# Kernel optimization log

Measured on AMD Instinct MI355X. Metric: run time of the kernel, lower is better.

The kernel has to match this reference:

```python
import jax, jax.numpy as jnp
import numpy as np

N_NODES = 50000
N_EDGES = 1_600_000
IN_DIM = 256
OUT_DIM = 128
NEG_SLOPE = 0.01  # F.leaky_relu default


def setup_inputs() -> dict:
    key = jax.random.key(0)
    k1, k2, k3, k4, k5 = jax.random.split(key, 5)
    x = jax.random.normal(k1, (N_NODES, IN_DIM), dtype=jnp.float32)
    # glorot_init: uniform in [-r, r], r = sqrt(6/(in+out))
    r = np.sqrt(6.0 / (IN_DIM + OUT_DIM)).astype(np.float32)
    weight = jax.random.uniform(k2, (IN_DIM, OUT_DIM), dtype=jnp.float32, minval=-r, maxval=r)
    adj_rows = jax.random.randint(k3, (N_EDGES,), 0, N_NODES, dtype=jnp.int64 if jax.config.jax_enable_x64 else jnp.int32)
    adj_cols = jax.random.randint(k4, (N_EDGES,), 0, N_NODES, dtype=jnp.int64 if jax.config.jax_enable_x64 else jnp.int32)
    adj_vals = jax.random.uniform(k5, (N_EDGES,), dtype=jnp.float32)
    return {"x": x, "weight": weight, "adj_vals": adj_vals,
            "adj_rows": adj_rows, "adj_cols": adj_cols}


def reference(x, weight, adj_vals, adj_rows, adj_cols):
    # h = X @ W : [N, OUT_DIM]
    h = x @ weight
    # sparse adj @ h via edge-list SpMM: out[r] += v * h[c]
    msgs = adj_vals[:, None] * h[adj_cols]            # [E, OUT_DIM]
    agg = jax.ops.segment_sum(msgs, adj_rows, num_segments=N_NODES)
    # leaky_relu epilogue
    return jnp.where(agg >= 0, agg, NEG_SLOPE * agg)
```

## Files before the change

### kernel.cpp

```cpp
#include <hip/hip_runtime.h>
#include <hip/hip_fp16.h>

#define N_NODES 50000
#define N_EDGES 1600000
#define IN_DIM 256
#define OUT_DIM 128
#define NEG_SLOPE 0.01f

#define SB_SH     10
#define SB_ROWS   1024
#define NSB       ((N_NODES + SB_ROWS - 1) / SB_ROWS)
#define SB_CAP    34816
#define PASSB_SPLIT 8
#define PB_ITERS  ((SB_CAP / PASSB_SPLIT + 511) / 512)

#define BIN_SH    5
#define BIN_ROWS  32
#define NBIN      ((N_NODES + BIN_ROWS - 1) / BIN_ROWS)
#define NBIN_PAD  (NSB * (SB_ROWS / BIN_ROWS))
#define CAPB      1280
#define OVF_CAP   65536

#define SCAT_BLOCKS 256
#define CONVW_BLOCKS 8
#define EPB_S (N_EDGES / SCAT_BLOCKS)
#define SCAT_ITERS ((EPB_S + 511) / 512)

typedef _Float16 f16x8 __attribute__((ext_vector_type(8)));
typedef float    f32x4 __attribute__((ext_vector_type(4)));
typedef float    f32x8 __attribute__((ext_vector_type(8)));

__device__ __forceinline__ float lrelu(float v) {
    return v >= 0.f ? v : NEG_SLOPE * v;
}

#define BM 128
#define GEMM_BLOCKS ((N_NODES + BM - 1) / BM)

#define CVT16(lo, hi) do { \
    lo[0]=(_Float16)xr[0].x; lo[1]=(_Float16)xr[0].y; lo[2]=(_Float16)xr[0].z; lo[3]=(_Float16)xr[0].w; \
    lo[4]=(_Float16)xr[1].x; lo[5]=(_Float16)xr[1].y; lo[6]=(_Float16)xr[1].z; lo[7]=(_Float16)xr[1].w; \
    hi[0]=(_Float16)xr[2].x; hi[1]=(_Float16)xr[2].y; hi[2]=(_Float16)xr[2].z; hi[3]=(_Float16)xr[2].w; \
    hi[4]=(_Float16)xr[3].x; hi[5]=(_Float16)xr[3].y; hi[6]=(_Float16)xr[3].z; hi[7]=(_Float16)xr[3].w; \
} while (0)

__global__ __launch_bounds__(256, 2) void gemm_xw_mfma(const float* __restrict__ x,
                                                       const __half* __restrict__ wtl,
                                                       __half* __restrict__ h) {
    __shared__ f16x8 wt8[32 * 128];
    __shared__ f16x8 xs8[2][4][BM];

    const int t    = threadIdx.x;
    const int lane = t & 63;
    const int wv   = t >> 6;
    const int row0 = blockIdx.x * BM;

    {
        const int4* src = (const int4*)wtl;
        int4* dst = (int4*)wt8;
#pragma unroll
        for (int i = 0; i < 16; ++i) dst[i * 256 + t] = src[i * 256 + t];
    }

    const int srow = t >> 1;
    const int skh  = t & 1;
    const int grow = row0 + srow;
    const bool rv  = grow < N_NODES;
    const float* xp = x + (size_t)(rv ? grow : 0) * IN_DIM + skh * 16;

    float4 xr[4];
#pragma unroll
    for (int i = 0; i < 4; ++i)
        xr[i] = rv ? ((const float4*)xp)[i] : make_float4(0.f, 0.f, 0.f, 0.f);
    {
        f16x8 lo, hi;
        CVT16(lo, hi);
        xs8[0][skh * 2 + 0][srow] = lo;
        xs8[0][skh * 2 + 1][srow] = hi;
    }
    __syncthreads();

    f32x4 acc[2][8];
#pragma unroll
    for (int mf = 0; mf < 2; ++mf)
#pragma unroll
        for (int nf = 0; nf < 8; ++nf) acc[mf][nf] = (f32x4){0.f, 0.f, 0.f, 0.f};

    const int kg  = lane >> 4;
    const int l15 = lane & 15;
    const int mb  = (wv << 5) + l15;

#pragma unroll
    for (int ks = 0; ks < 8; ++ks) {
        const int cur = ks & 1;
        if (ks < 7) {
#pragma unroll
            for (int i = 0; i < 4; ++i)
                xr[i] = rv ? ((const float4*)(xp + (ks + 1) * 32))[i]
                           : make_float4(0.f, 0.f, 0.f, 0.f);
        }
        const f16x8 b0 = xs8[cur][kg][mb];
        const f16x8 b1 = xs8[cur][kg][mb + 16];
#pragma unroll
        for (int nf = 0; nf < 8; ++nf) {
            const f16x8 a = wt8[(((ks << 2) | kg) << 7) + (nf << 4) + l15];
            acc[0][nf] = __builtin_amdgcn_mfma_f32_16x16x32_f16(a, b0, acc[0][nf], 0, 0, 0);
            acc[1][nf] = __builtin_amdgcn_mfma_f32_16x16x32_f16(a, b1, acc[1][nf], 0, 0, 0);
        }
        if (ks < 7) {
            f16x8 lo, hi;
            CVT16(lo, hi);
            xs8[cur ^ 1][skh * 2 + 0][srow] = lo;
            xs8[cur ^ 1][skh * 2 + 1][srow] = hi;
            __syncthreads();
        }
    }

    const int rg = lane >> 4;
#pragma unroll
    for (int mf = 0; mf < 2; ++mf) {
        const int m = row0 + (wv << 5) + (mf << 4) + l15;
        if (m < N_NODES) {
            __half* hp = h + (size_t)m * OUT_DIM + (rg << 2);
#pragma unroll
            for (int nf = 0; nf < 8; ++nf) {
                union { ushort4 u; __half f[4]; } o;
                o.f[0] = __float2half(acc[mf][nf][0]);
                o.f[1] = __float2half(acc[mf][nf][1]);
                o.f[2] = __float2half(acc[mf][nf][2]);
                o.f[3] = __float2half(acc[mf][nf][3]);
                *(ushort4*)(hp + (nf << 4)) = o.u;
            }
        }
    }
}

__global__ __launch_bounds__(512) void scatter_coarse(const int* __restrict__ rows,
                                                      const int* __restrict__ cols,
                                                      const float* __restrict__ vals,
                                                      int* __restrict__ sbcur,
                                                      int* __restrict__ ovfcnt,
                                                      int2* __restrict__ cbuf,
                                                      int2* __restrict__ ovfbuf,
                                                      const float* __restrict__ w,
                                                      __half* __restrict__ wtl) {
    if (blockIdx.x >= SCAT_BLOCKS) {
        const int e0 = ((blockIdx.x - SCAT_BLOCKS) * 512 + threadIdx.x) * 8;
        const int k  = e0 >> 7;
        const int n0 = e0 & 127;
        const float4 a = *(const float4*)(w + e0);
        const float4 b = *(const float4*)(w + e0 + 4);
        __half* dst = wtl + ((size_t)((k >> 3) * 128 + n0)) * 8 + (k & 7);
        dst[0]  = __float2half(a.x);
        dst[8]  = __float2half(a.y);
        dst[16] = __float2half(a.z);
        dst[24] = __float2half(a.w);
        dst[32] = __float2half(b.x);
        dst[40] = __float2half(b.y);
        dst[48] = __float2half(b.z);
        dst[56] = __float2half(b.w);
        return;
    }

    __shared__ int lcur[NSB];
    const int t = threadIdx.x;
    const int ebase = blockIdx.x * EPB_S;

    if (t < NSB) lcur[t] = 0;
    __syncthreads();

    int myr[SCAT_ITERS];
#pragma unroll
    for (int k = 0; k < SCAT_ITERS; ++k) {
        const int i = k * 512 + t;
        myr[k] = -1;
        if (i < EPB_S) {
            const int r = rows[ebase + i];
            myr[k] = r;
            atomicAdd(&lcur[r >> SB_SH], 1);
        }
    }
    __syncthreads();

    if (t < NSB) {
        const int c = lcur[t];
        lcur[t] = (c > 0) ? atomicAdd(&sbcur[t], c) : 0;
    }
    __syncthreads();

#pragma unroll
    for (int k = 0; k < SCAT_ITERS; ++k) {
        const int i = k * 512 + t;
        if (i < EPB_S) {
            const int e = ebase + i;
            const int r = myr[k];
            const int sb = r >> SB_SH;
            const int off = atomicAdd(&lcur[sb], 1);
            const int key = (int)(((unsigned)r << 16) | (unsigned)cols[e]);
            const int vb  = __float_as_int(vals[e]);
            if (off < SB_CAP) {
                cbuf[(size_t)sb * SB_CAP + off] = make_int2(key, vb);
            } else {
                const int p = atomicAdd(ovfcnt, 1);
                if (p < OVF_CAP) ovfbuf[p] = make_int2(key, vb);
            }
        }
    }
}

__global__ __launch_bounds__(512) void scatter_fine(const int* __restrict__ sbcur,
                                                    int* __restrict__ fcur,
                                                    int* __restrict__ ovfcnt,
                                                    const int2* __restrict__ cbuf,
                                                    int2* __restrict__ ebuf,
                                                    int2* __restrict__ ovfbuf) {
    __shared__ int lcur[SB_ROWS / BIN_ROWS];
    const int t    = threadIdx.x;
    const int sb   = blockIdx.x / PASSB_SPLIT;
    const int part = blockIdx.x % PASSB_SPLIT;

    const int cnt_sb = min(sbcur[sb], SB_CAP);
    const int chunk  = (cnt_sb + PASSB_SPLIT - 1) / PASSB_SPLIT;
    const int i0 = part * chunk;
    const int i1 = min(i0 + chunk, cnt_sb);

    if (t < 32) lcur[t] = 0;
    __syncthreads();

    int2 rc[PB_ITERS];
#pragma unroll
    for (int k = 0; k < PB_ITERS; ++k) {
        const int i = i0 + k * 512 + t;
        if (i < i1) {
            rc[k] = cbuf[(size_t)sb * SB_CAP + i];
            const unsigned urow = ((unsigned)rc[k].x) >> 16;
            atomicAdd(&lcur[(urow >> BIN_SH) & 31], 1);
        }
    }
    __syncthreads();

    if (t < 32) {
        const int c = lcur[t];
        lcur[t] = (c > 0) ? atomicAdd(&fcur[(sb << 5) + t], c) : 0;
    }
    __syncthreads();

#pragma unroll
    for (int k = 0; k < PB_ITERS; ++k) {
        const int i = i0 + k * 512 + t;
        if (i < i1) {
            const unsigned urow = ((unsigned)rc[k].x) >> 16;
            const int f   = (int)(urow >> BIN_SH);
            const int off = atomicAdd(&lcur[(urow >> BIN_SH) & 31], 1);
            const int key = (rc[k].x & 0xFFFF) | (int)((urow & (BIN_ROWS - 1)) << 16);
            if (off < CAPB) {
                ebuf[(size_t)f * CAPB + off] = make_int2(key, rc[k].y);
            } else {
                const int p = atomicAdd(ovfcnt, 1);
                if (p < OVF_CAP) ovfbuf[p] = rc[k];
            }
        }
    }
}

#define NCLS 256

__global__ __launch_bounds__(512) void sort_gather(const int* __restrict__ fcur,
                                                   const int* __restrict__ ovfcnt,
                                                   const int2* __restrict__ ebuf,
                                                   const int2* __restrict__ ovfbuf,
                                                   const __half* __restrict__ h,
                                                   float* __restrict__ out) {
    __shared__ int2 srec[CAPB];
    __shared__ int  hist[NCLS];
    __shared__ int  pfx[NCLS];
    __shared__ int  rowoff_l[BIN_ROWS + 1];

    const int t    = threadIdx.x;
    const int bin  = blockIdx.x;
    const int wv   = t >> 6;
    const int lane = t & 63;

    const int cnt_all = fcur[bin];
    const int cnt     = cnt_all < CAPB ? cnt_all : CAPB;
    const size_t base = (size_t)bin * CAPB;

    if (t < NCLS) hist[t] = 0;
    __syncthreads();

    for (int i = t; i < cnt; i += 512) {
        const int k = ebuf[base + i].x;
        atomicAdd(&hist[(((k >> 16) & 31) << 3) | ((k & 0xFFFF) >> 13)], 1);
    }
    __syncthreads();

    if (t < NCLS) pfx[t] = hist[t];
    __syncthreads();
    for (int off = 1; off < NCLS; off <<= 1) {
        const int u = (t >= off && t < NCLS) ? pfx[t - off] : 0;
        __syncthreads();
        if (t < NCLS) pfx[t] += u;
        __syncthreads();
    }
    if (t < NCLS) hist[t] = pfx[t] - hist[t];
    if (t < BIN_ROWS) rowoff_l[t] = t ? pfx[(t << 3) - 1] : 0;
    if (t == BIN_ROWS) rowoff_l[BIN_ROWS] = cnt;
    __syncthreads();

    for (int i = t; i < cnt; i += 512) {
        const int2 r = ebuf[base + i];
        const int cls = (((r.x >> 16) & 31) << 3) | ((r.x & 0xFFFF) >> 13);
        const int pos = atomicAdd(&hist[cls], 1);
        srec[pos] = r;
    }
    __syncthreads();

    const int grp = lane >> 4;
    const int gl  = lane & 15;
    int novf = *ovfcnt;
    if (novf > OVF_CAP) novf = OVF_CAP;

    for (int p = 0; p < 2; ++p) {
        const int lr0 = (wv << 2) + 2 * p;
        const int lr1 = lr0 + 1;
        const int b0 = rowoff_l[lr0], e0 = rowoff_l[lr0 + 1];
        const int b1 = rowoff_l[lr1], e1 = rowoff_l[lr1 + 1];
        const int n0 = e0 - b0, n1 = e1 - b1;
        const int nmax = n0 > n1 ? n0 : n1;
        const int iters = (nmax + 3) >> 2;

        f32x8 a0 = (f32x8){0.f,0.f,0.f,0.f,0.f,0.f,0.f,0.f};
        f32x8 a1 = (f32x8){0.f,0.f,0.f,0.f,0.f,0.f,0.f,0.f};

        for (int it = 0; it < iters; ++it) {
            const int i0 = b0 + (it << 2) + grp;
            const int i1 = b1 + (it << 2) + grp;
            const bool v0i = i0 < e0;
            const bool v1i = i1 < e1;
            const int2 rA = srec[v0i ? i0 : 0];
            const int2 rB = srec[v1i ? i1 : 0];
            const float vA = v0i ? __int_as_float(rA.y) : 0.f;
            const float vB = v1i ? __int_as_float(rB.y) : 0.f;
            const f16x8 hA = *(const f16x8*)(h + (size_t)(rA.x & 0xFFFF) * OUT_DIM + (gl << 3));
            const f16x8 hB = *(const f16x8*)(h + (size_t)(rB.x & 0xFFFF) * OUT_DIM + (gl << 3));
#pragma unroll
            for (int j = 0; j < 8; ++j) {
                a0[j] += vA * (float)hA[j];
                a1[j] += vB * (float)hB[j];
            }
        }

        for (int e = 0; e < novf; ++e) {
            const int2 rec = ovfbuf[e];
            const unsigned urow = ((unsigned)rec.x) >> 16;
            if ((int)(urow >> BIN_SH) == bin && grp == 0) {
                const int lrow = (int)(urow & (BIN_ROWS - 1));
                if (lrow == lr0 || lrow == lr1) {
                    const float v = __int_as_float(rec.y);
                    const f16x8 hv = *(const f16x8*)(h + (size_t)(rec.x & 0xFFFF) * OUT_DIM + (gl << 3));
#pragma unroll
                    for (int j = 0; j < 8; ++j) {
                        if (lrow == lr0) a0[j] += v * (float)hv[j];
                        else             a1[j] += v * (float)hv[j];
                    }
                }
            }
        }

#pragma unroll
        for (int j = 0; j < 8; ++j) {
            float x0 = a0[j], x1 = a1[j];
            x0 += __shfl_xor(x0, 16); x0 += __shfl_xor(x0, 32);
            x1 += __shfl_xor(x1, 16); x1 += __shfl_xor(x1, 32);
            a0[j] = x0; a1[j] = x1;
        }

        const int lrow = (grp & 2) ? lr1 : lr0;
        const int grow = (bin << BIN_SH) + lrow;
        float q[4];
#pragma unroll
        for (int k = 0; k < 4; ++k) {
            const float lo = (grp & 2) ? a1[k]     : a0[k];
            const float hi = (grp & 2) ? a1[k + 4] : a0[k + 4];
            q[k] = lrelu((grp & 1) ? hi : lo);
        }
        if (grow < N_NODES) {
            float4 o = make_float4(q[0], q[1], q[2], q[3]);
            *(float4*)(out + (size_t)grow * OUT_DIM + (gl << 3) + ((grp & 1) << 2)) = o;
        }
    }
}

extern "C" void kernel_launch(void* const* d_in, const int* in_sizes, int n_in,
                              void* d_out, int out_size, void* d_ws, size_t ws_size,
                              hipStream_t stream) {
    const float* x    = (const float*)d_in[0];
    const float* w    = (const float*)d_in[1];
    const float* vals = (const float*)d_in[2];
    const int*   rows = (const int*)d_in[3];
    const int*   cols = (const int*)d_in[4];
    float* out = (float*)d_out;

    char* ws = (char*)d_ws;
    size_t off = 0;
    auto alloc = [&](size_t bytes) {
        void* p = ws + off;
        off = (off + bytes + 255) & ~(size_t)255;
        return p;
    };
    int2*  cbuf    = (int2*) alloc((size_t)NSB * SB_CAP * sizeof(int2));
    __half* h      = (__half*)cbuf;
    int2*  ebuf    = (int2*) alloc((size_t)NBIN * CAPB * sizeof(int2));
    int2*  ovfbuf  = (int2*) alloc((size_t)OVF_CAP * sizeof(int2));
    __half* wtl    = (__half*)alloc((size_t)IN_DIM * OUT_DIM * sizeof(__half));
    int*   meta    = (int*)  alloc((size_t)(NSB + NBIN_PAD + 1) * sizeof(int));
    int*   sbcur   = meta;
    int*   fcur    = meta + NSB;
    int*   ovfcnt  = meta + NSB + NBIN_PAD;

    hipMemsetAsync(meta, 0, (size_t)(NSB + NBIN_PAD + 1) * sizeof(int), stream);

    scatter_coarse<<<SCAT_BLOCKS + CONVW_BLOCKS, 512, 0, stream>>>(rows, cols, vals,
                                                                   sbcur, ovfcnt, cbuf, ovfbuf, w, wtl);
    scatter_fine<<<NSB * PASSB_SPLIT, 512, 0, stream>>>(sbcur, fcur, ovfcnt, cbuf, ebuf, ovfbuf);
    gemm_xw_mfma<<<GEMM_BLOCKS, 256, 0, stream>>>(x, wtl, h);
    sort_gather<<<NBIN, 512, 0, stream>>>(fcur, ovfcnt, ebuf, ovfbuf, h, out);
}
```

Baseline: 200.6 us.

## Process four rows per wave with software-prefetched gathers in sort_gather

The sort_gather kernel now stages each bin's edge records in shared memory once instead of reading them from global memory twice. It replaces the block-wide Hillis-Steele scan with a wave-shuffle scan. The gather loop handles all four rows of a wave at once, and the fp16 h-row loads are double-buffered so the next iteration's loads are in flight during the current FMAs. This aims to hide gather latency and cut synchronisation and redundant global reads. In exchange it uses more registers and about 10KB more LDS, under a launch bound of 4 blocks.

```diff
diff --git a/kernel.cpp b/kernel.cpp
--- a/kernel.cpp
+++ b/kernel.cpp
@@ -265,16 +265,29 @@
 
 #define NCLS 256
 
-__global__ __launch_bounds__(512) void sort_gather(const int* __restrict__ fcur,
-                                                   const int* __restrict__ ovfcnt,
-                                                   const int2* __restrict__ ebuf,
-                                                   const int2* __restrict__ ovfbuf,
-                                                   const __half* __restrict__ h,
-                                                   float* __restrict__ out) {
+#define STAGE(IT, HV, VV) do {                                                  \
+    _Pragma("unroll")                                                           \
+    for (int q = 0; q < 4; ++q) {                                               \
+        const int idx = beg[q] + ((IT) << 2) + grp;                             \
+        const bool vld = idx < end[q];                                          \
+        const int2 r = srec[vld ? idx : 0];                                     \
+        VV[q] = vld ? __int_as_float(r.y) : 0.f;                                \
+        HV[q] = *(const f16x8*)(h + (size_t)(r.x & 0xFFFF) * OUT_DIM + (gl << 3)); \
+    }                                                                           \
+} while (0)
+
+__global__ __launch_bounds__(512, 4) void sort_gather(const int* __restrict__ fcur,
+                                                      const int* __restrict__ ovfcnt,
+                                                      const int2* __restrict__ ebuf,
+                                                      const int2* __restrict__ ovfbuf,
+                                                      const __half* __restrict__ h,
+                                                      float* __restrict__ out) {
+    __shared__ int2 urec[CAPB];
     __shared__ int2 srec[CAPB];
     __shared__ int  hist[NCLS];
     __shared__ int  pfx[NCLS];
     __shared__ int  rowoff_l[BIN_ROWS + 1];
+    __shared__ int  wsum[4];
 
     const int t    = threadIdx.x;
     const int bin  = blockIdx.x;
@@ -289,26 +302,41 @@
     __syncthreads();
 
     for (int i = t; i < cnt; i += 512) {
-        const int k = ebuf[base + i].x;
-        atomicAdd(&hist[(((k >> 16) & 31) << 3) | ((k & 0xFFFF) >> 13)], 1);
-    }
-    __syncthreads();
-
-    if (t < NCLS) pfx[t] = hist[t];
-    __syncthreads();
-    for (int off = 1; off < NCLS; off <<= 1) {
-        const int u = (t >= off && t < NCLS) ? pfx[t - off] : 0;
+        const int2 r = ebuf[base + i];
+        urec[i] = r;
+        atomicAdd(&hist[(((r.x >> 16) & 31) << 3) | ((r.x & 0xFFFF) >> 13)], 1);
+    }
+    __syncthreads();
+
+    {
+        const int v = (t < NCLS) ? hist[t] : 0;
+        int s = v;
+#pragma unroll
+        for (int off = 1; off < 64; off <<= 1) {
+            const int u = __shfl_up(s, off);
+            if (lane >= off) s += u;
+        }
+        if (t < NCLS && lane == 63) wsum[wv] = s;
         __syncthreads();
-        if (t < NCLS) pfx[t] += u;
+        if (t == 0) {
+            int a = 0;
+#pragma unroll
+            for (int i = 0; i < 4; ++i) { const int c = wsum[i]; wsum[i] = a; a += c; }
+        }
         __syncthreads();
-    }
-    if (t < NCLS) hist[t] = pfx[t] - hist[t];
+        if (t < NCLS) {
+            const int incl = s + wsum[wv];
+            pfx[t]  = incl;
+            hist[t] = incl - v;
+        }
+    }
+    __syncthreads();
     if (t < BIN_ROWS) rowoff_l[t] = t ? pfx[(t << 3) - 1] : 0;
     if (t == BIN_ROWS) rowoff_l[BIN_ROWS] = cnt;
     __syncthreads();
 
     for (int i = t; i < cnt; i += 512) {
-        const int2 r = ebuf[base + i];
+        const int2 r = urec[i];
         const int cls = (((r.x >> 16) & 31) << 3) | ((r.x & 0xFFFF) >> 13);
         const int pos = atomicAdd(&hist[cls], 1);
         srec[pos] = r;
@@ -317,77 +345,76 @@
 
     const int grp = lane >> 4;
     const int gl  = lane & 15;
+    const int r0  = wv << 2;
+
+    int beg[4], end[4];
+#pragma unroll
+    for (int q = 0; q < 4; ++q) { beg[q] = rowoff_l[r0 + q]; end[q] = rowoff_l[r0 + q + 1]; }
+    int nmax = 0;
+#pragma unroll
+    for (int q = 0; q < 4; ++q) nmax = max(nmax, end[q] - beg[q]);
+    const int iters = (nmax + 3) >> 2;
+
+    f32x8 acc[4];
+#pragma unroll
+    for (int q = 0; q < 4; ++q) acc[q] = (f32x8){0.f,0.f,0.f,0.f,0.f,0.f,0.f,0.f};
+
+    f16x8 hc[4], hn[4];
+    float vc[4], vn[4];
+    if (iters > 0) STAGE(0, hc, vc);
+    for (int it = 0; it < iters; ++it) {
+        if (it + 1 < iters) STAGE(it + 1, hn, vn);
+#pragma unroll
+        for (int q = 0; q < 4; ++q)
+#pragma unroll
+            for (int j = 0; j < 8; ++j) acc[q][j] += vc[q] * (float)hc[q][j];
+#pragma unroll
+        for (int q = 0; q < 4; ++q) { hc[q] = hn[q]; vc[q] = vn[q]; }
+    }
+
     int novf = *ovfcnt;
     if (novf > OVF_CAP) novf = OVF_CAP;
-
-    for (int p = 0; p < 2; ++p) {
-        const int lr0 = (wv << 2) + 2 * p;
-        const int lr1 = lr0 + 1;
-        const int b0 = rowoff_l[lr0], e0 = rowoff_l[lr0 + 1];
-        const int b1 = rowoff_l[lr1], e1 = rowoff_l[lr1 + 1];
-        const int n0 = e0 - b0, n1 = e1 - b1;
-        const int nmax = n0 > n1 ? n0 : n1;
-        const int iters = (nmax + 3) >> 2;
-
-        f32x8 a0 = (f32x8){0.f,0.f,0.f,0.f,0.f,0.f,0.f,0.f};
-        f32x8 a1 = (f32x8){0.f,0.f,0.f,0.f,0.f,0.f,0.f,0.f};
-
-        for (int it = 0; it < iters; ++it) {
-            const int i0 = b0 + (it << 2) + grp;
-            const int i1 = b1 + (it << 2) + grp;
-            const bool v0i = i0 < e0;
-            const bool v1i = i1 < e1;
-            const int2 rA = srec[v0i ? i0 : 0];
-            const int2 rB = srec[v1i ? i1 : 0];
-            const float vA = v0i ? __int_as_float(rA.y) : 0.f;
-            const float vB = v1i ? __int_as_float(rB.y) : 0.f;
-            const f16x8 hA = *(const f16x8*)(h + (size_t)(rA.x & 0xFFFF) * OUT_DIM + (gl << 3));
-            const f16x8 hB = *(const f16x8*)(h + (size_t)(rB.x & 0xFFFF) * OUT_DIM + (gl << 3));
-#pragma unroll
-            for (int j = 0; j < 8; ++j) {
-                a0[j] += vA * (float)hA[j];
-                a1[j] += vB * (float)hB[j];
+    for (int e = 0; e < novf; ++e) {
+        const int2 rec = ovfbuf[e];
+        const unsigned urow = ((unsigned)rec.x) >> 16;
+        if ((int)(urow >> BIN_SH) == bin && grp == 0) {
+            const int lr = (int)(urow & (BIN_ROWS - 1)) - r0;
+            if (lr >= 0 && lr < 4) {
+                const float v = __int_as_float(rec.y);
+                const f16x8 hv = *(const f16x8*)(h + (size_t)(rec.x & 0xFFFF) * OUT_DIM + (gl << 3));
+#pragma unroll
+                for (int q = 0; q < 4; ++q)
+                    if (q == lr)
+#pragma unroll
+                        for (int j = 0; j < 8; ++j) acc[q][j] += v * (float)hv[j];
             }
         }
-
-        for (int e = 0; e < novf; ++e) {
-            const int2 rec = ovfbuf[e];
-            const unsigned urow = ((unsigned)rec.x) >> 16;
-            if ((int)(urow >> BIN_SH) == bin && grp == 0) {
-                const int lrow = (int)(urow & (BIN_ROWS - 1));
-                if (lrow == lr0 || lrow == lr1) {
-                    const float v = __int_as_float(rec.y);
-                    const f16x8 hv = *(const f16x8*)(h + (size_t)(rec.x & 0xFFFF) * OUT_DIM + (gl << 3));
-#pragma unroll
-                    for (int j = 0; j < 8; ++j) {
-                        if (lrow == lr0) a0[j] += v * (float)hv[j];
-                        else             a1[j] += v * (float)hv[j];
-                    }
-                }
-            }
-        }
-
+    }
+
+#pragma unroll
+    for (int q = 0; q < 4; ++q)
 #pragma unroll
         for (int j = 0; j < 8; ++j) {
-            float x0 = a0[j], x1 = a1[j];
-            x0 += __shfl_xor(x0, 16); x0 += __shfl_xor(x0, 32);
-            x1 += __shfl_xor(x1, 16); x1 += __shfl_xor(x1, 32);
-            a0[j] = x0; a1[j] = x1;
-        }
-
-        const int lrow = (grp & 2) ? lr1 : lr0;
-        const int grow = (bin << BIN_SH) + lrow;
-        float q[4];
-#pragma unroll
-        for (int k = 0; k < 4; ++k) {
-            const float lo = (grp & 2) ? a1[k]     : a0[k];
-            const float hi = (grp & 2) ? a1[k + 4] : a0[k + 4];
-            q[k] = lrelu((grp & 1) ? hi : lo);
-        }
-        if (grow < N_NODES) {
-            float4 o = make_float4(q[0], q[1], q[2], q[3]);
-            *(float4*)(out + (size_t)grow * OUT_DIM + (gl << 3) + ((grp & 1) << 2)) = o;
-        }
+            float x = acc[q][j];
+            x += __shfl_xor(x, 16);
+            x += __shfl_xor(x, 32);
+            acc[q][j] = x;
+        }
+
+    float res[8];
+#pragma unroll
+    for (int j = 0; j < 8; ++j) {
+        float x = acc[0][j];
+        x = (grp == 1) ? acc[1][j] : x;
+        x = (grp == 2) ? acc[2][j] : x;
+        x = (grp == 3) ? acc[3][j] : x;
+        res[j] = lrelu(x);
+    }
+    const int grow = (bin << BIN_SH) + r0 + grp;
+    if (grow < N_NODES) {
+        float* op = out + (size_t)grow * OUT_DIM + (gl << 3);
+        *(float4*)op       = make_float4(res[0], res[1], res[2], res[3]);
+        *(float4*)(op + 4) = make_float4(res[4], res[5], res[6], res[7]);
     }
 }
 
```

Result: slower. 205.4 us (+2.4%).
